# Kernel optimization log

Measured on AMD Instinct MI355X. Metric: run time of the kernel, lower is better.

## Reference

```python
import jax, jax.numpy as jnp
import numpy as np

NUM_HEADS = 4

def setup_inputs() -> dict:
    key = jax.random.key(0)
    ks = jax.random.split(key, 8)
    B, C, H, W = 4, 256, 128, 128
    Cq = C // 8  # query/key channels
    x  = jax.random.normal(ks[0], (B, C, H, W), dtype=jnp.float32)
    Wq = jax.random.normal(ks[1], (Cq, C), dtype=jnp.float32) * 0.05
    bq = jax.random.normal(ks[2], (Cq,),  dtype=jnp.float32) * 0.01
    Wk = jax.random.normal(ks[3], (Cq, C), dtype=jnp.float32) * 0.05
    bk = jax.random.normal(ks[4], (Cq,),  dtype=jnp.float32) * 0.01
    Wv = jax.random.normal(ks[5], (C, C),  dtype=jnp.float32) * 0.05
    bv = jax.random.normal(ks[6], (C,),   dtype=jnp.float32) * 0.01
    # torch init is zeros; use a nonzero value so the attention path contributes
    gamma = jnp.array([0.5], dtype=jnp.float32)
    return {"x": x, "Wq": Wq, "bq": bq, "Wk": Wk, "bk": bk, "Wv": Wv, "bv": bv, "gamma": gamma}

def _conv1x1(x, Wm, b):
    # 1x1 conv == per-pixel linear map over channels
    return jnp.einsum('bchw,oc->bohw', x, Wm) + b[None, :, None, None]

def reference(x, Wq, bq, Wk, bk, Wv, bv, gamma):
    B, C, H, W = x.shape
    nh = NUM_HEADS
    # project, then fold heads into batch: (B*nh, c_head, H, W)
    q = _conv1x1(x, Wq, bq).reshape(B * nh, -1, H, W)
    k = _conv1x1(x, Wk, bk).reshape(B * nh, -1, H, W)
    v = _conv1x1(x, Wv, bv).reshape(B * nh, -1, H, W)
    # horizontal (row-wise) attention over W: energy [BH, H, W, W]
    e_h = jnp.einsum('bchw,bchv->bhwv', q, k)
    a_h = jax.nn.softmax(e_h, axis=-1)
    o_h = jnp.einsum('bhwv,bchv->bchw', a_h, v)  # (BH, cv, H, W)
    # vertical (column-wise) attention over H: energy [BH, W, H, H]
    e_v = jnp.einsum('bchw,bcgw->bwhg', q, k)
    a_v = jax.nn.softmax(e_v, axis=-1)
    # original permutes back as (BH, cv, W, H); requires H == W to add
    o_v = jnp.einsum('bwhg,bcgw->bcwh', a_v, v)
    attn = (o_h + o_v).reshape(B, C, H, W)
    return gamma * attn + x
```

## Files before the change

kernel.cpp:

```cpp
#include <hip/hip_runtime.h>

#define HW 16384

typedef __attribute__((ext_vector_type(8))) short short8;
typedef __attribute__((ext_vector_type(16))) float floatx16;

__device__ inline unsigned short f2bf(float f) {
    unsigned u = __builtin_bit_cast(unsigned, f);
    u = (u + 0x7FFFu + ((u >> 16) & 1u)) >> 16;
    return (unsigned short)u;
}

__device__ inline unsigned pack_bf_trunc(float lo, float hi) {
    return __builtin_amdgcn_perm(__builtin_bit_cast(unsigned, hi),
                                 __builtin_bit_cast(unsigned, lo), 0x07060302u);
}

__global__ __launch_bounds__(256) void castW_kernel(
    const float* __restrict__ Wq, const float* __restrict__ Wk,
    const float* __restrict__ Wv, unsigned short* __restrict__ Wb)
{
    int idx4 = blockIdx.x * 256 + threadIdx.x;
    int e0 = idx4 * 4;
    int row = e0 >> 8, col = e0 & 255;
    const float* src = (row < 32) ? (Wq + row * 256 + col)
                     : (row < 64) ? (Wk + (row - 32) * 256 + col)
                                  : (Wv + (row - 64) * 256 + col);
    float4 v = *(const float4*)src;
    uint2 pk;
    pk.x = f2bf(v.x) | ((unsigned)f2bf(v.y) << 16);
    pk.y = f2bf(v.z) | ((unsigned)f2bf(v.w) << 16);
    *(uint2*)&Wb[e0] = pk;
}

__global__ __launch_bounds__(256) void cast_xt_kernel(
    const float* __restrict__ x, unsigned short* __restrict__ xt)
{
    __shared__ unsigned short T[64][66];
    const int tid = threadIdx.x;
    const int p0 = blockIdx.x * 64;
    const int c0 = blockIdx.y * 64;
    const int b  = blockIdx.z;
    #pragma unroll
    for (int i = 0; i < 4; i++) {
        int e = i * 256 + tid;
        int c = e >> 4, seg = e & 15;
        float4 v = *(const float4*)&x[((b * 256 + c0 + c) << 14) + p0 + seg * 4];
        ((unsigned*)&T[c][seg * 4])[0] = f2bf(v.x) | ((unsigned)f2bf(v.y) << 16);
        ((unsigned*)&T[c][seg * 4])[1] = f2bf(v.z) | ((unsigned)f2bf(v.w) << 16);
    }
    __syncthreads();
    #pragma unroll
    for (int i = 0; i < 2; i++) {
        int e = i * 256 + tid;
        int p = e >> 3, cs = e & 7;
        unsigned short t[8];
        #pragma unroll
        for (int j = 0; j < 8; j++) t[j] = T[cs * 8 + j][p];
        uint4 pk;
        pk.x = t[0] | ((unsigned)t[1] << 16);
        pk.y = t[2] | ((unsigned)t[3] << 16);
        pk.z = t[4] | ((unsigned)t[5] << 16);
        pk.w = t[6] | ((unsigned)t[7] << 16);
        *(uint4*)&xt[(((b << 14) + p0 + p) << 8) + c0 + cs * 8] = pk;
    }
}

__global__ __launch_bounds__(256, 3) void proj_mfma_kernel(
    const unsigned short* __restrict__ Wb, const unsigned short* __restrict__ xt,
    const float* __restrict__ bq, const float* __restrict__ bk,
    const float* __restrict__ bv,
    unsigned short* __restrict__ qb, unsigned short* __restrict__ kb,
    unsigned short* __restrict__ vb)
{
    __shared__ __align__(16) unsigned short As[64 * 64];
    __shared__ __align__(16) unsigned short Bs[256 * 64];
    __shared__ float biasS[64];
    const int tid = threadIdx.x;
    const int p0  = blockIdx.x * 256;
    const int oc0 = blockIdx.y * 64;
    const int b   = blockIdx.z;
    const int w = tid >> 6, lr = tid & 31, lh = (tid & 63) >> 5;

    if (tid < 64) biasS[tid] = (oc0 == 0) ? ((tid < 32) ? bq[tid] : bk[tid - 32])
                                          : bv[oc0 - 64 + tid];

    floatx16 z16 = {0,0,0,0,0,0,0,0,0,0,0,0,0,0,0,0};
    floatx16 acc[2][2] = {{z16, z16}, {z16, z16}};
    const int bpx = (b << 14) + p0;

    for (int kc = 0; kc < 256; kc += 64) {
        if (kc) __syncthreads();
        #pragma unroll
        for (int i = 0; i < 2; i++) {
            int e = i * 256 + tid;
            int row = e >> 3, seg = e & 7, cp = seg ^ (row & 7);
            *(uint4*)&As[row * 64 + cp * 8] =
                *(const uint4*)&Wb[(oc0 + row) * 256 + kc + seg * 8];
        }
        #pragma unroll
        for (int i = 0; i < 8; i++) {
            int e = i * 256 + tid;
            int row = e >> 3, seg = e & 7, cp = seg ^ (row & 7);
            *(uint4*)&Bs[row * 64 + cp * 8] =
                *(const uint4*)&xt[((bpx + row) << 8) + kc + seg * 8];
        }
        __syncthreads();
        #pragma unroll
        for (int ks = 0; ks < 4; ks++) {
            int c = 2 * ks + lh;
            int cx = (c ^ (lr & 7)) * 8;
            short8 af0 = *(const short8*)&As[lr * 64 + cx];
            short8 af1 = *(const short8*)&As[(32 + lr) * 64 + cx];
            short8 bf0 = *(const short8*)&Bs[(64 * w + lr) * 64 + cx];
            short8 bf1 = *(const short8*)&Bs[(64 * w + 32 + lr) * 64 + cx];
            acc[0][0] = __builtin_amdgcn_mfma_f32_32x32x16_bf16(af0, bf0, acc[0][0], 0, 0, 0);
            acc[0][1] = __builtin_amdgcn_mfma_f32_32x32x16_bf16(af0, bf1, acc[0][1], 0, 0, 0);
            acc[1][0] = __builtin_amdgcn_mfma_f32_32x32x16_bf16(af1, bf0, acc[1][0], 0, 0, 0);
            acc[1][1] = __builtin_amdgcn_mfma_f32_32x32x16_bf16(af1, bf1, acc[1][1], 0, 0, 0);
        }
    }

    __syncthreads();
    if (oc0 == 0) {
        unsigned short* Cq = Bs;
        #pragma unroll
        for (int i = 0; i < 2; i++) {
            #pragma unroll
            for (int j = 0; j < 2; j++) {
                int px = 64 * w + 32 * j + lr;
                #pragma unroll
                for (int g = 0; g < 4; g++) {
                    float v0 = acc[i][j][4*g+0] + biasS[32*i + 8*g + 4*lh + 0];
                    float v1 = acc[i][j][4*g+1] + biasS[32*i + 8*g + 4*lh + 1];
                    float v2 = acc[i][j][4*g+2] + biasS[32*i + 8*g + 4*lh + 2];
                    float v3 = acc[i][j][4*g+3] + biasS[32*i + 8*g + 4*lh + 3];
                    uint2 u; u.x = pack_bf_trunc(v0, v1); u.y = pack_bf_trunc(v2, v3);
                    int cp = (4 * i + g) ^ (px & 7);
                    *(uint2*)&Cq[px * 64 + cp * 8 + 4 * lh] = u;
                }
            }
        }
        __syncthreads();
        #pragma unroll
        for (int i = 0; i < 8; i++) {
            int px = tid;
            int cp = i ^ (px & 7);
            uint4 val = *(const uint4*)&Cq[px * 64 + cp * 8];
            if (i < 4) *(uint4*)&qb[(unsigned)((b * 4 + i)     * HW + p0 + px) * 8] = val;
            else       *(uint4*)&kb[(unsigned)((b * 4 + i - 4) * HW + p0 + px) * 8] = val;
        }
    } else {
        unsigned short* Cv = Bs;
        #pragma unroll
        for (int i = 0; i < 2; i++) {
            #pragma unroll
            for (int j = 0; j < 2; j++) {
                int px = 64 * w + 32 * j + lr;
                #pragma unroll
                for (int reg = 0; reg < 16; reg++) {
                    int oc = 32 * i + (reg & 3) + 8 * (reg >> 2) + 4 * lh;
                    float v = acc[i][j][reg] + biasS[oc];
                    int cp = (px >> 3) ^ (oc & 31);
                    Cv[oc * 256 + cp * 8 + (px & 7)] =
                        (unsigned short)(__builtin_bit_cast(unsigned, v) >> 16);
                }
            }
        }
        __syncthreads();
        #pragma unroll
        for (int i = 0; i < 8; i++) {
            int u = i * 256 + tid;
            int oc = u >> 5, seg = u & 31;
            int cp = seg ^ (oc & 31);
            uint4 val = *(const uint4*)&Cv[oc * 256 + cp * 8];
            *(uint4*)&vb[(unsigned)(b * 256 + oc0 - 64 + oc) * HW + p0 + seg * 8] = val;
        }
    }
}

__global__ __launch_bounds__(256) void tqk_kernel(
    const unsigned short* __restrict__ qb, const unsigned short* __restrict__ kb,
    unsigned short* __restrict__ qt, unsigned short* __restrict__ kt)
{
    __shared__ uint4 t[32][33];
    const int plane = blockIdx.y;
    const int tile  = blockIdx.x;
    const int tx = tile & 3, ty = tile >> 2;
    const uint4* src = (const uint4*)(plane < 16 ? qb : kb) + (plane & 15) * HW;
    uint4*       dst = (uint4*)(plane < 16 ? qt : kt) + (plane & 15) * HW;
    const int c = threadIdx.x & 31, r0 = threadIdx.x >> 5;
    #pragma unroll
    for (int i = 0; i < 4; i++) {
        int r = r0 + i * 8;
        t[r][c] = src[(ty * 32 + r) * 128 + tx * 32 + c];
    }
    __syncthreads();
    #pragma unroll
    for (int i = 0; i < 4; i++) {
        int r = r0 + i * 8;
        dst[(tx * 32 + r) * 128 + ty * 32 + c] = t[c][r];
    }
}

__global__ __launch_bounds__(256) void tv_kernel(
    const unsigned short* __restrict__ vb, unsigned short* __restrict__ vt)
{
    __shared__ unsigned short T[64][66];
    const int plane = blockIdx.y;
    const int tile  = blockIdx.x;
    const int tx = tile & 1, ty = tile >> 1;
    const unsigned* src = (const unsigned*)(vb + plane * HW);
    unsigned*       dst = (unsigned*)(vt + plane * HW);
    const int tid = threadIdx.x;
    #pragma unroll
    for (int i = 0; i < 8; i++) {
        int e = i * 256 + tid;
        int r = e >> 5, cp = e & 31;
        *(unsigned*)&T[r][2 * cp] = src[(ty * 64 + r) * 64 + tx * 32 + cp];
    }
    __syncthreads();
    #pragma unroll
    for (int i = 0; i < 8; i++) {
        int e = i * 256 + tid;
        int c = e >> 5, rp = e & 31;
        unsigned lo = T[2 * rp][c], hi = T[2 * rp + 1][c];
        dst[(tx * 64 + c) * 64 + ty * 32 + rp] = lo | (hi << 16);
    }
}

__global__ __launch_bounds__(256, 3) void attn_kernel(
    const unsigned short* __restrict__ qb, const unsigned short* __restrict__ kb,
    const unsigned short* __restrict__ vb,
    const unsigned short* __restrict__ qt, const unsigned short* __restrict__ kt,
    const unsigned short* __restrict__ vt,
    const float* __restrict__ xin, const float* __restrict__ gamma,
    float* __restrict__ out)
{
    __shared__ __align__(16) unsigned short Vs[64 * 128];
    __shared__ __align__(16) unsigned short Ps[128 * 128];
    __shared__ float red[4][128];

    const int tid = threadIdx.x;
    const int y = blockIdx.x, bh = blockIdx.y;
    const int w = tid >> 6, l = tid & 63, lr = l & 31, lh = l >> 5;
    const float L2E = 1.4426950408889634f;

    floatx16 z16 = {0,0,0,0,0,0,0,0,0,0,0,0,0,0,0,0};
    floatx16 o0 = z16, o1 = z16;
    short8 z8 = {0,0,0,0,0,0,0,0};

    for (int stage = 0; stage < 2; stage++) {
        const unsigned short* qsrc = (stage ? qt : qb) + (bh * 128 + y) * 1024;
        const unsigned short* ksrc = (stage ? kt : kb) + (bh * 128 + y) * 1024;
        const unsigned short* vsrc = stage ? vt : vb;
        if (stage) __syncthreads();
        #pragma unroll
        for (int i = 0; i < 4; i++) {
            int e = i * 256 + tid;
            int ch = e >> 4, sg = e & 15;
            int sgp = sg ^ (ch & 15);
            *(uint4*)&Vs[ch * 128 + sgp * 8] =
                *(const uint4*)(vsrc + (bh * 64 + ch) * HW + y * 128 + sg * 8);
        }
        short8 af = z8;
        short8 bf[4] = {z8, z8, z8, z8};
        if (lh == 0) {
            af = *(const short8*)(ksrc + (32 * w + lr) * 8);
            #pragma unroll
            for (int nt = 0; nt < 4; nt++)
                bf[nt] = *(const short8*)(qsrc + (32 * nt + lr) * 8);
        }
        floatx16 et[4];
        #pragma unroll
        for (int nt = 0; nt < 4; nt++)
            et[nt] = __builtin_amdgcn_mfma_f32_32x32x16_bf16(af, bf[nt], z16, 0, 0, 0);

        #pragma unroll
        for (int nt = 0; nt < 4; nt++) {
            float s = 0.f;
            #pragma unroll
            for (int r = 0; r < 16; r++) {
                float p = exp2f(et[nt][r] * L2E);
                et[nt][r] = p;
                s += p;
            }
            s += __shfl_xor(s, 32);
            if (lh == 0) red[w][32 * nt + lr] = s;
        }
        __syncthreads();
        float rl[4];
        #pragma unroll
        for (int nt = 0; nt < 4; nt++) {
            int q = 32 * nt + lr;
            rl[nt] = 1.0f / (red[0][q] + red[1][q] + red[2][q] + red[3][q]);
        }
        #pragma unroll
        for (int nt = 0; nt < 4; nt++) {
            int row = 32 * nt + lr;
            #pragma unroll
            for (int g = 0; g < 4; g++) {
                uint2 u;
                u.x = pack_bf_trunc(et[nt][4*g+0] * rl[nt], et[nt][4*g+1] * rl[nt]);
                u.y = pack_bf_trunc(et[nt][4*g+2] * rl[nt], et[nt][4*g+3] * rl[nt]);
                int cp = (4 * w + g) ^ (lr & 15);
                *(uint2*)&Ps[row * 128 + cp * 8 + 4 * lh] = u;
            }
        }
        __syncthreads();
        #pragma unroll
        for (int ks = 0; ks < 8; ks++) {
            int cp = ((2 * ks + lh) ^ (lr & 15)) * 8;
            short8 pf = *(const short8*)&Ps[(32 * w + lr) * 128 + cp];
            short8 v0 = *(const short8*)&Vs[lr * 128 + cp];
            short8 v1 = *(const short8*)&Vs[(32 + lr) * 128 + cp];
            o0 = __builtin_amdgcn_mfma_f32_32x32x16_bf16(v0, pf, o0, 0, 0, 0);
            o1 = __builtin_amdgcn_mfma_f32_32x32x16_bf16(v1, pf, o1, 0, 0, 0);
        }
    }

    const float g = gamma[0];
    const int xq = 32 * w + lr;
    #pragma unroll
    for (int reg = 0; reg < 16; reg++) {
        int ch = (reg & 3) + 8 * (reg >> 2) + 4 * lh;
        int idx0 = (bh * 64 + ch) * HW + y * 128 + xq;
        int idx1 = (bh * 64 + 32 + ch) * HW + y * 128 + xq;
        out[idx0] = g * o0[reg] + xin[idx0];
        out[idx1] = g * o1[reg] + xin[idx1];
    }
}

extern "C" void kernel_launch(void* const* d_in, const int* in_sizes, int n_in,
                              void* d_out, int out_size, void* d_ws, size_t ws_size,
                              hipStream_t stream) {
    const float* x     = (const float*)d_in[0];
    const float* Wq    = (const float*)d_in[1];
    const float* bq    = (const float*)d_in[2];
    const float* Wk    = (const float*)d_in[3];
    const float* bk    = (const float*)d_in[4];
    const float* Wv    = (const float*)d_in[5];
    const float* bv    = (const float*)d_in[6];
    const float* gamma = (const float*)d_in[7];
    float* out = (float*)d_out;

    unsigned short* Wb   = (unsigned short*)d_ws;
    unsigned short* qb16 = Wb + 320 * 256;
    unsigned short* kb16 = qb16 + 16 * HW * 8;
    unsigned short* qt16 = kb16 + 16 * HW * 8;
    unsigned short* kt16 = qt16 + 16 * HW * 8;
    unsigned short* vb16 = kt16 + 16 * HW * 8;
    unsigned short* vt16 = vb16 + 1024 * HW;
    unsigned short* xt = (unsigned short*)d_out;

    castW_kernel<<<dim3(80), 256, 0, stream>>>(Wq, Wk, Wv, Wb);
    cast_xt_kernel<<<dim3(256, 4, 4), 256, 0, stream>>>(x, xt);
    proj_mfma_kernel<<<dim3(64, 5, 4), 256, 0, stream>>>(Wb, xt, bq, bk, bv, qb16, kb16, vb16);
    tqk_kernel<<<dim3(16, 32), 256, 0, stream>>>(qb16, kb16, qt16, kt16);
    tv_kernel<<<dim3(4, 1024), 256, 0, stream>>>(vb16, vt16);
    attn_kernel<<<dim3(128, 16), 256, 0, stream>>>(qb16, kb16, vb16, qt16, kt16, vt16, x, gamma, out);
}
```

Measured before the change: 202.2 us.

## Keep softmax probabilities in registers and defer normalization in attention kernel

The attention kernel now computes the energy transposed so each wave owns full query rows. Unnormalized exp probabilities stay in registers as packed bf16 and are exchanged between lane halves with shuffles to form the MFMA B operand. This removes the Ps shared buffer, the cross-wave reduction array and two barriers per stage. Normalization is deferred: the first stage's accumulator is rescaled by l1/l0 and the final output is scaled by gamma/l1. Both V tiles are loaded up front into double shared buffers and occupancy is raised to 4 blocks, at the cost of more register pressure and slightly different rounding from normalizing after the bf16 cast.

Result: slower. 208.6 us (+3.1%).

```diff
diff --git a/kernel.cpp b/kernel.cpp
--- a/kernel.cpp
+++ b/kernel.cpp
@@ -229,7 +229,7 @@
     }
 }
 
-__global__ __launch_bounds__(256, 3) void attn_kernel(
+__global__ __launch_bounds__(256, 4) void attn_kernel(
     const unsigned short* __restrict__ qb, const unsigned short* __restrict__ kb,
     const unsigned short* __restrict__ vb,
     const unsigned short* __restrict__ qt, const unsigned short* __restrict__ kt,
@@ -237,97 +237,143 @@
     const float* __restrict__ xin, const float* __restrict__ gamma,
     float* __restrict__ out)
 {
-    __shared__ __align__(16) unsigned short Vs[64 * 128];
-    __shared__ __align__(16) unsigned short Ps[128 * 128];
-    __shared__ float red[4][128];
+    __shared__ __align__(16) unsigned short Vs[2][64 * 128];
 
     const int tid = threadIdx.x;
     const int y = blockIdx.x, bh = blockIdx.y;
-    const int w = tid >> 6, l = tid & 63, lr = l & 31, lh = l >> 5;
+    const int w = tid >> 6, l = tid & 63, lr = l & 31;
+    const bool lhi = (l & 32) != 0;
     const float L2E = 1.4426950408889634f;
 
     floatx16 z16 = {0,0,0,0,0,0,0,0,0,0,0,0,0,0,0,0};
     floatx16 o0 = z16, o1 = z16;
     short8 z8 = {0,0,0,0,0,0,0,0};
 
-    for (int stage = 0; stage < 2; stage++) {
-        const unsigned short* qsrc = (stage ? qt : qb) + (bh * 128 + y) * 1024;
-        const unsigned short* ksrc = (stage ? kt : kb) + (bh * 128 + y) * 1024;
-        const unsigned short* vsrc = stage ? vt : vb;
-        if (stage) __syncthreads();
+    #pragma unroll
+    for (int st = 0; st < 2; st++) {
+        const unsigned short* vsrc = st ? vt : vb;
         #pragma unroll
         for (int i = 0; i < 4; i++) {
             int e = i * 256 + tid;
             int ch = e >> 4, sg = e & 15;
             int sgp = sg ^ (ch & 15);
-            *(uint4*)&Vs[ch * 128 + sgp * 8] =
+            *(uint4*)&Vs[st][ch * 128 + sgp * 8] =
                 *(const uint4*)(vsrc + (bh * 64 + ch) * HW + y * 128 + sg * 8);
         }
-        short8 af = z8;
-        short8 bf[4] = {z8, z8, z8, z8};
-        if (lh == 0) {
-            af = *(const short8*)(ksrc + (32 * w + lr) * 8);
-            #pragma unroll
-            for (int nt = 0; nt < 4; nt++)
-                bf[nt] = *(const short8*)(qsrc + (32 * nt + lr) * 8);
-        }
-        floatx16 et[4];
-        #pragma unroll
-        for (int nt = 0; nt < 4; nt++)
-            et[nt] = __builtin_amdgcn_mfma_f32_32x32x16_bf16(af, bf[nt], z16, 0, 0, 0);
-
-        #pragma unroll
-        for (int nt = 0; nt < 4; nt++) {
-            float s = 0.f;
-            #pragma unroll
-            for (int r = 0; r < 16; r++) {
-                float p = exp2f(et[nt][r] * L2E);
-                et[nt][r] = p;
-                s += p;
+    }
+
+    uint2 pk[4][4];
+
+    const unsigned short* q0 = qb + (bh * 128 + y) * 1024;
+    const unsigned short* k0 = kb + (bh * 128 + y) * 1024;
+    float l0 = 0.f;
+    {
+        short8 bf = z8, af[4] = {z8, z8, z8, z8};
+        if (!lhi) {
+            bf = *(const short8*)(q0 + (32 * w + lr) * 8);
+            #pragma unroll
+            for (int kblk = 0; kblk < 4; kblk++)
+                af[kblk] = *(const short8*)(k0 + (32 * kblk + lr) * 8);
+        }
+        #pragma unroll
+        for (int kblk = 0; kblk < 4; kblk++) {
+            floatx16 et = __builtin_amdgcn_mfma_f32_32x32x16_bf16(af[kblk], bf, z16, 0, 0, 0);
+            #pragma unroll
+            for (int g = 0; g < 4; g++) {
+                float p0 = exp2f(et[4*g+0] * L2E);
+                float p1 = exp2f(et[4*g+1] * L2E);
+                float p2 = exp2f(et[4*g+2] * L2E);
+                float p3 = exp2f(et[4*g+3] * L2E);
+                l0 += (p0 + p1) + (p2 + p3);
+                pk[kblk][g].x = pack_bf_trunc(p0, p1);
+                pk[kblk][g].y = pack_bf_trunc(p2, p3);
             }
-            s += __shfl_xor(s, 32);
-            if (lh == 0) red[w][32 * nt + lr] = s;
-        }
-        __syncthreads();
-        float rl[4];
-        #pragma unroll
-        for (int nt = 0; nt < 4; nt++) {
-            int q = 32 * nt + lr;
-            rl[nt] = 1.0f / (red[0][q] + red[1][q] + red[2][q] + red[3][q]);
-        }
-        #pragma unroll
-        for (int nt = 0; nt < 4; nt++) {
-            int row = 32 * nt + lr;
+        }
+    }
+    l0 += __shfl_xor(l0, 32);
+
+    __syncthreads();
+
+    #pragma unroll
+    for (int ks = 0; ks < 8; ks++) {
+        int kblk = ks >> 1, h2 = ks & 1;
+        uint2 a = pk[kblk][2 * h2], b2 = pk[kblk][2 * h2 + 1];
+        unsigned ownx = lhi ? b2.x : a.x,  owny = lhi ? b2.y : a.y;
+        unsigned sndx = lhi ? a.x  : b2.x, sndy = lhi ? a.y  : b2.y;
+        unsigned rcx = (unsigned)__shfl_xor((int)sndx, 32);
+        unsigned rcy = (unsigned)__shfl_xor((int)sndy, 32);
+        uint4 uu;
+        uu.x = lhi ? rcx : ownx;  uu.y = lhi ? rcy : owny;
+        uu.z = lhi ? ownx : rcx;  uu.w = lhi ? owny : rcy;
+        short8 pf = __builtin_bit_cast(short8, uu);
+        int cp = ((2 * ks + (lhi ? 1 : 0)) ^ (lr & 15)) * 8;
+        short8 v0 = *(const short8*)&Vs[0][lr * 128 + cp];
+        short8 v1 = *(const short8*)&Vs[0][(32 + lr) * 128 + cp];
+        o0 = __builtin_amdgcn_mfma_f32_32x32x16_bf16(v0, pf, o0, 0, 0, 0);
+        o1 = __builtin_amdgcn_mfma_f32_32x32x16_bf16(v1, pf, o1, 0, 0, 0);
+    }
+
+    const unsigned short* q1 = qt + (bh * 128 + y) * 1024;
+    const unsigned short* k1 = kt + (bh * 128 + y) * 1024;
+    float l1 = 0.f;
+    {
+        short8 bf = z8, af[4] = {z8, z8, z8, z8};
+        if (!lhi) {
+            bf = *(const short8*)(q1 + (32 * w + lr) * 8);
+            #pragma unroll
+            for (int kblk = 0; kblk < 4; kblk++)
+                af[kblk] = *(const short8*)(k1 + (32 * kblk + lr) * 8);
+        }
+        #pragma unroll
+        for (int kblk = 0; kblk < 4; kblk++) {
+            floatx16 et = __builtin_amdgcn_mfma_f32_32x32x16_bf16(af[kblk], bf, z16, 0, 0, 0);
             #pragma unroll
             for (int g = 0; g < 4; g++) {
-                uint2 u;
-                u.x = pack_bf_trunc(et[nt][4*g+0] * rl[nt], et[nt][4*g+1] * rl[nt]);
-                u.y = pack_bf_trunc(et[nt][4*g+2] * rl[nt], et[nt][4*g+3] * rl[nt]);
-                int cp = (4 * w + g) ^ (lr & 15);
-                *(uint2*)&Ps[row * 128 + cp * 8 + 4 * lh] = u;
+                float p0 = exp2f(et[4*g+0] * L2E);
+                float p1 = exp2f(et[4*g+1] * L2E);
+                float p2 = exp2f(et[4*g+2] * L2E);
+                float p3 = exp2f(et[4*g+3] * L2E);
+                l1 += (p0 + p1) + (p2 + p3);
+                pk[kblk][g].x = pack_bf_trunc(p0, p1);
+                pk[kblk][g].y = pack_bf_trunc(p2, p3);
             }
         }
-        __syncthreads();
-        #pragma unroll
-        for (int ks = 0; ks < 8; ks++) {
-            int cp = ((2 * ks + lh) ^ (lr & 15)) * 8;
-            short8 pf = *(const short8*)&Ps[(32 * w + lr) * 128 + cp];
-            short8 v0 = *(const short8*)&Vs[lr * 128 + cp];
-            short8 v1 = *(const short8*)&Vs[(32 + lr) * 128 + cp];
-            o0 = __builtin_amdgcn_mfma_f32_32x32x16_bf16(v0, pf, o0, 0, 0, 0);
-            o1 = __builtin_amdgcn_mfma_f32_32x32x16_bf16(v1, pf, o1, 0, 0, 0);
-        }
-    }
-
-    const float g = gamma[0];
+    }
+    l1 += __shfl_xor(l1, 32);
+
+    float s01 = l1 / l0;
+    #pragma unroll
+    for (int r = 0; r < 16; r++) { o0[r] *= s01; o1[r] *= s01; }
+
+    #pragma unroll
+    for (int ks = 0; ks < 8; ks++) {
+        int kblk = ks >> 1, h2 = ks & 1;
+        uint2 a = pk[kblk][2 * h2], b2 = pk[kblk][2 * h2 + 1];
+        unsigned ownx = lhi ? b2.x : a.x,  owny = lhi ? b2.y : a.y;
+        unsigned sndx = lhi ? a.x  : b2.x, sndy = lhi ? a.y  : b2.y;
+        unsigned rcx = (unsigned)__shfl_xor((int)sndx, 32);
+        unsigned rcy = (unsigned)__shfl_xor((int)sndy, 32);
+        uint4 uu;
+        uu.x = lhi ? rcx : ownx;  uu.y = lhi ? rcy : owny;
+        uu.z = lhi ? ownx : rcx;  uu.w = lhi ? owny : rcy;
+        short8 pf = __builtin_bit_cast(short8, uu);
+        int cp = ((2 * ks + (lhi ? 1 : 0)) ^ (lr & 15)) * 8;
+        short8 v0 = *(const short8*)&Vs[1][lr * 128 + cp];
+        short8 v1 = *(const short8*)&Vs[1][(32 + lr) * 128 + cp];
+        o0 = __builtin_amdgcn_mfma_f32_32x32x16_bf16(v0, pf, o0, 0, 0, 0);
+        o1 = __builtin_amdgcn_mfma_f32_32x32x16_bf16(v1, pf, o1, 0, 0, 0);
+    }
+
+    const float c = gamma[0] / l1;
+    const int lh = lhi ? 1 : 0;
     const int xq = 32 * w + lr;
     #pragma unroll
     for (int reg = 0; reg < 16; reg++) {
         int ch = (reg & 3) + 8 * (reg >> 2) + 4 * lh;
         int idx0 = (bh * 64 + ch) * HW + y * 128 + xq;
         int idx1 = (bh * 64 + 32 + ch) * HW + y * 128 + xq;
-        out[idx0] = g * o0[reg] + xin[idx0];
-        out[idx1] = g * o1[reg] + xin[idx1];
+        out[idx0] = c * o0[reg] + xin[idx0];
+        out[idx1] = c * o1[reg] + xin[idx1];
     }
 }
 
```
